# Optimization experiments

Measured on AMD Instinct MI355X. Metric: run time of the kernel, lower is better.

Reference implementation:

```python
import jax, jax.numpy as jnp
import numpy as np

B, L, IN_SIZE, EMB = 1024, 128, 64, 256
N_HEADS = 4
GAT_HID, GAT_HEADS = 64, 4
GAT_OUT = GAT_HEADS * GAT_HID  # 256 (concat=True)
NUM_CLASSES = 16
N_EDGES = 16384
NEG_SLOPE = 0.2


def layer_norm(x, g, b, eps=1e-5):
    mu = x.mean(-1, keepdims=True)
    var = x.var(-1, keepdims=True)
    return (x - mu) / jnp.sqrt(var + eps) * g + b


def mha(x, pad_mask, wqkv, bqkv, wo, bo):
    # torch nn.MultiheadAttention (batch_first), eval mode -> dropout is identity
    Bs, Ls, Em = x.shape
    dh = Em // N_HEADS
    qkv = x @ wqkv + bqkv                                   # [B,L,3E]
    q, k, v = jnp.split(qkv, 3, axis=-1)
    q = q.reshape(Bs, Ls, N_HEADS, dh)
    k = k.reshape(Bs, Ls, N_HEADS, dh)
    v = v.reshape(Bs, Ls, N_HEADS, dh)
    scores = jnp.einsum('bqhd,bkhd->bhqk', q, k) * (1.0 / np.sqrt(dh))
    scores = jnp.where(pad_mask[:, None, None, :], jnp.asarray(-1e9, scores.dtype), scores)
    attn = jax.nn.softmax(scores, axis=-1)
    out = jnp.einsum('bhqk,bkhd->bqhd', attn, v).reshape(Bs, Ls, Em)
    return out @ wo + bo


def gat_conv(h, src, dst, w, a_src, a_dst, bias):
    # PyG GATConv: per-node linear, additive attention, segment softmax over
    # incoming edges (grouped by dst), scatter-add aggregation, concat heads.
    N = h.shape[0]
    xh = (h @ w).reshape(N, GAT_HEADS, -1)                  # [N,H,F]
    s = (xh * a_src).sum(-1)                                # [N,H]
    d = (xh * a_dst).sum(-1)                                # [N,H]
    e = s[src] + d[dst]                                     # [E,H]
    e = jnp.where(e > 0, e, NEG_SLOPE * e)                  # leaky_relu(0.2)
    emax = jax.ops.segment_max(e, dst, num_segments=N)      # per-dst max
    ee = jnp.exp(e - emax[dst])
    denom = jax.ops.segment_sum(ee, dst, num_segments=N)
    coef = ee / (denom[dst] + 1e-16)                        # [E,H]
    msg = xh[src] * coef[:, :, None]                        # [E,H,F]
    out = jax.ops.segment_sum(msg, dst, num_segments=N)     # [N,H,F]
    return out.reshape(N, -1) + bias


def setup_inputs():
    key = jax.random.key(0)
    ks = jax.random.split(key, 16)
    rn = lambda i, shape, fan: jax.random.normal(ks[i], shape, jnp.float32) / np.sqrt(fan)
    inp = {}
    inp['x'] = jax.random.normal(ks[0], (B, L, IN_SIZE), jnp.float32)
    inp['lengths'] = jax.random.randint(ks[1], (B,), 1, L + 1)
    inp['edge_index'] = jax.random.randint(ks[2], (2, N_EDGES), 0, B)
    inp['in_w'] = rn(3, (IN_SIZE, EMB), IN_SIZE)
    inp['in_b'] = jnp.zeros((EMB,), jnp.float32)
    inp['mha1_wqkv'] = rn(4, (EMB, 3 * EMB), EMB)
    inp['mha1_bqkv'] = jnp.zeros((3 * EMB,), jnp.float32)
    inp['mha1_wo'] = rn(5, (EMB, EMB), EMB)
    inp['mha1_bo'] = jnp.zeros((EMB,), jnp.float32)
    inp['mha2_wqkv'] = rn(6, (EMB, 3 * EMB), EMB)
    inp['mha2_bqkv'] = jnp.zeros((3 * EMB,), jnp.float32)
    inp['mha2_wo'] = rn(7, (EMB, EMB), EMB)
    inp['mha2_bo'] = jnp.zeros((EMB,), jnp.float32)
    inp['ln1_g'] = jnp.ones((EMB,), jnp.float32)
    inp['ln1_b'] = jnp.zeros((EMB,), jnp.float32)
    inp['ln2_g'] = jnp.ones((EMB,), jnp.float32)
    inp['ln2_b'] = jnp.zeros((EMB,), jnp.float32)
    inp['gat1_w'] = rn(8, (EMB, GAT_OUT), EMB)
    inp['gat1_asrc'] = rn(9, (GAT_HEADS, GAT_HID), GAT_HID)
    inp['gat1_adst'] = rn(10, (GAT_HEADS, GAT_HID), GAT_HID)
    inp['gat1_bias'] = jnp.zeros((GAT_OUT,), jnp.float32)
    inp['gat2_w'] = rn(11, (GAT_OUT, GAT_OUT), GAT_OUT)
    inp['gat2_asrc'] = rn(12, (GAT_HEADS, GAT_HID), GAT_HID)
    inp['gat2_adst'] = rn(13, (GAT_HEADS, GAT_HID), GAT_HID)
    inp['gat2_bias'] = jnp.zeros((GAT_OUT,), jnp.float32)
    inp['lng1_g'] = jnp.ones((GAT_OUT,), jnp.float32)
    inp['lng1_b'] = jnp.zeros((GAT_OUT,), jnp.float32)
    inp['lng2_g'] = jnp.ones((GAT_OUT,), jnp.float32)
    inp['lng2_b'] = jnp.zeros((GAT_OUT,), jnp.float32)
    inp['fc_w'] = rn(14, (GAT_OUT, NUM_CLASSES), GAT_OUT)
    inp['fc_b'] = jnp.zeros((NUM_CLASSES,), jnp.float32)
    return inp


def reference(x, lengths, edge_index, in_w, in_b,
              mha1_wqkv, mha1_bqkv, mha1_wo, mha1_bo,
              mha2_wqkv, mha2_bqkv, mha2_wo, mha2_bo,
              ln1_g, ln1_b, ln2_g, ln2_b,
              gat1_w, gat1_asrc, gat1_adst, gat1_bias,
              gat2_w, gat2_asrc, gat2_adst, gat2_bias,
              lng1_g, lng1_b, lng2_g, lng2_b, fc_w, fc_b):
    pad_mask = jnp.arange(L)[None, :] >= lengths[:, None]   # True = padding
    h = x @ in_w + in_b                                     # [B,L,EMB]
    h = layer_norm(h + mha(h, pad_mask, mha1_wqkv, mha1_bqkv, mha1_wo, mha1_bo), ln1_g, ln1_b)
    h = layer_norm(h + mha(h, pad_mask, mha2_wqkv, mha2_bqkv, mha2_wo, mha2_bo), ln2_g, ln2_b)
    valid = (~pad_mask)[:, :, None].astype(h.dtype)
    pooled = (h * valid).sum(1) / jnp.clip(lengths, 1, None)[:, None].astype(h.dtype)  # [B,EMB]
    src, dst = edge_index[0], edge_index[1]
    g = gat_conv(pooled, src, dst, gat1_w, gat1_asrc, gat1_adst, gat1_bias)
    g = jax.nn.relu(layer_norm(g, lng1_g, lng1_b))
    g = gat_conv(g, src, dst, gat2_w, gat2_asrc, gat2_adst, gat2_bias)
    g = jax.nn.relu(layer_norm(g, lng2_g, lng2_b))
    return g @ fc_w + fc_b
```

## Files before the change

### kernel.cpp

```cpp
#include <hip/hip_runtime.h>
#include <hip/hip_bf16.h>
#include <cstdint>
#include <cstddef>

#define B_SZ    1024
#define L_SEQ   128
#define INSZ    64
#define EMB     256
#define NH      4
#define DH      64
#define QKV3    768
#define NEDGE   16384
#define GHEADS  4
#define GHID    64
#define GOUT    256
#define NCLS    16

#define NCHUNK     8
#define BCHUNK     (B_SZ / NCHUNK)
#define ROWS_CHUNK (BCHUNK * L_SEQ)

typedef unsigned short ushort_t;
typedef short bf16x8 __attribute__((ext_vector_type(8)));
typedef float f32x4 __attribute__((ext_vector_type(4)));
typedef ushort_t us4 __attribute__((ext_vector_type(4)));
typedef ushort_t us8 __attribute__((ext_vector_type(8)));

__device__ __forceinline__ ushort_t f32_to_bf16_rne(float x) {
    unsigned u = __float_as_uint(x);
    unsigned r = u + 0x7FFFu + ((u >> 16) & 1u);
    return (ushort_t)(r >> 16);
}
__device__ __forceinline__ float bf16u_to_f32(ushort_t h) {
    return __uint_as_float(((unsigned)h) << 16);
}

__global__ __launch_bounds__(256) void wsplit_kernel(
    const float* __restrict__ W, ushort_t* __restrict__ WtH,
    ushort_t* __restrict__ WtL, int K, int N)
{
    const int t = blockIdx.x * 256 + threadIdx.x;
    if (t >= K * N) return;
    const int n = t / K, k = t - n * K;
    const float x = W[(size_t)k * N + n];
    const ushort_t hi = f32_to_bf16_rne(x);
    const ushort_t lo = f32_to_bf16_rne(x - bf16u_to_f32(hi));
    WtH[t] = hi;
    WtL[t] = lo;
}

#define AKP 40

__global__ __launch_bounds__(256) void gemm_mfma_split(
    const float* __restrict__ A, const ushort_t* __restrict__ BtH,
    const ushort_t* __restrict__ BtL, const float* __restrict__ bias,
    float* __restrict__ C, int K, int lda, int ldc)
{
    __shared__ __attribute__((aligned(16))) ushort_t AsH[128][AKP];
    __shared__ __attribute__((aligned(16))) ushort_t AsL[128][AKP];
    __shared__ __attribute__((aligned(16))) ushort_t BsH[128][AKP];
    __shared__ __attribute__((aligned(16))) ushort_t BsL[128][AKP];

    const int tid  = threadIdx.x;
    const int lane = tid & 63;
    const int wv   = tid >> 6;
    const int wm   = (wv >> 1) << 6;
    const int wn   = (wv & 1) << 6;
    const int fr   = lane & 15;
    const int fk   = (lane >> 4) << 3;
    const size_t brow = (size_t)blockIdx.y << 7;
    const int    bcol = blockIdx.x << 7;

    const int ar = tid >> 3;
    const int ac = (tid & 7) << 2;
    const int bn = tid >> 1;
    const int bk = (tid & 1) << 4;

    f32x4 acc[4][4] = {};

    for (int k0 = 0; k0 < K; k0 += 32) {
        #pragma unroll
        for (int rr = 0; rr < 4; ++rr) {
            const int row = ar + (rr << 5);
            const float4 v = *reinterpret_cast<const float4*>(
                &A[(brow + row) * lda + k0 + ac]);
            const ushort_t h0 = f32_to_bf16_rne(v.x);
            const ushort_t h1 = f32_to_bf16_rne(v.y);
            const ushort_t h2 = f32_to_bf16_rne(v.z);
            const ushort_t h3 = f32_to_bf16_rne(v.w);
            const ushort_t l0 = f32_to_bf16_rne(v.x - bf16u_to_f32(h0));
            const ushort_t l1 = f32_to_bf16_rne(v.y - bf16u_to_f32(h1));
            const ushort_t l2 = f32_to_bf16_rne(v.z - bf16u_to_f32(h2));
            const ushort_t l3 = f32_to_bf16_rne(v.w - bf16u_to_f32(h3));
            us4 hv = {h0, h1, h2, h3};
            us4 lv = {l0, l1, l2, l3};
            *reinterpret_cast<us4*>(&AsH[row][ac]) = hv;
            *reinterpret_cast<us4*>(&AsL[row][ac]) = lv;
        }
        {
            const size_t bb = (size_t)(bcol + bn) * K + k0 + bk;
            *reinterpret_cast<us8*>(&BsH[bn][bk]) =
                *reinterpret_cast<const us8*>(&BtH[bb]);
            *reinterpret_cast<us8*>(&BsH[bn][bk + 8]) =
                *reinterpret_cast<const us8*>(&BtH[bb + 8]);
            *reinterpret_cast<us8*>(&BsL[bn][bk]) =
                *reinterpret_cast<const us8*>(&BtL[bb]);
            *reinterpret_cast<us8*>(&BsL[bn][bk + 8]) =
                *reinterpret_cast<const us8*>(&BtL[bb + 8]);
        }
        __syncthreads();

        bf16x8 aH[4], aL[4], bH[4], bL[4];
        #pragma unroll
        for (int i = 0; i < 4; ++i) {
            aH[i] = *reinterpret_cast<const bf16x8*>(&AsH[wm + (i << 4) + fr][fk]);
            aL[i] = *reinterpret_cast<const bf16x8*>(&AsL[wm + (i << 4) + fr][fk]);
            bH[i] = *reinterpret_cast<const bf16x8*>(&BsH[wn + (i << 4) + fr][fk]);
            bL[i] = *reinterpret_cast<const bf16x8*>(&BsL[wn + (i << 4) + fr][fk]);
        }
        #pragma unroll
        for (int i = 0; i < 4; ++i) {
            #pragma unroll
            for (int j = 0; j < 4; ++j) {
                acc[i][j] = __builtin_amdgcn_mfma_f32_16x16x32_bf16(
                    aH[i], bH[j], acc[i][j], 0, 0, 0);
                acc[i][j] = __builtin_amdgcn_mfma_f32_16x16x32_bf16(
                    aL[i], bH[j], acc[i][j], 0, 0, 0);
                acc[i][j] = __builtin_amdgcn_mfma_f32_16x16x32_bf16(
                    aH[i], bL[j], acc[i][j], 0, 0, 0);
            }
        }
        __syncthreads();
    }

    const int r4 = (lane >> 4) << 2;
    #pragma unroll
    for (int j = 0; j < 4; ++j) {
        const int col = bcol + wn + (j << 4) + fr;
        const float bv = bias ? bias[col] : 0.f;
        #pragma unroll
        for (int i = 0; i < 4; ++i) {
            #pragma unroll
            for (int r = 0; r < 4; ++r) {
                const size_t row = brow + wm + (i << 4) + r4 + r;
                C[row * ldc + col] = acc[i][j][r] + bv;
            }
        }
    }
}

#define BM 64
#define BN 64
#define BK 32

__global__ __launch_bounds__(256) void gemm_bias(
    const float* __restrict__ A, const float* __restrict__ Bm,
    const float* __restrict__ bias, float* __restrict__ C,
    int M, int N, int K, int lda, int ldb, int ldc)
{
    __shared__ float As[BK][BM + 4];
    __shared__ float Bs[BK][BN];
    const int tid = threadIdx.x;
    const int tx = tid & 15, ty = tid >> 4;
    const int brow = blockIdx.y * BM, bcol = blockIdx.x * BN;

    float acc[4][4] = {{0.f, 0.f, 0.f, 0.f}, {0.f, 0.f, 0.f, 0.f},
                       {0.f, 0.f, 0.f, 0.f}, {0.f, 0.f, 0.f, 0.f}};

    for (int k0 = 0; k0 < K; k0 += BK) {
        {
            const int r  = tid >> 3;
            const int c4 = (tid & 7) << 2;
            #pragma unroll
            for (int rr = 0; rr < 2; ++rr) {
                const int row = r + (rr << 5);
                const float4 v = *reinterpret_cast<const float4*>(
                    &A[(size_t)(brow + row) * lda + k0 + c4]);
                As[c4 + 0][row] = v.x;
                As[c4 + 1][row] = v.y;
                As[c4 + 2][row] = v.z;
                As[c4 + 3][row] = v.w;
            }
        }
        {
            const int r  = tid >> 4;
            const int c4 = tx << 2;
            #pragma unroll
            for (int rr = 0; rr < 2; ++rr) {
                const int row = r + (rr << 4);
                *reinterpret_cast<float4*>(&Bs[row][c4]) =
                    *reinterpret_cast<const float4*>(
                        &Bm[(size_t)(k0 + row) * ldb + bcol + c4]);
            }
        }
        __syncthreads();
        #pragma unroll
        for (int k = 0; k < BK; ++k) {
            const float4 av = *reinterpret_cast<const float4*>(&As[k][ty << 2]);
            const float4 bv = *reinterpret_cast<const float4*>(&Bs[k][tx << 2]);
            acc[0][0] += av.x * bv.x; acc[0][1] += av.x * bv.y;
            acc[0][2] += av.x * bv.z; acc[0][3] += av.x * bv.w;
            acc[1][0] += av.y * bv.x; acc[1][1] += av.y * bv.y;
            acc[1][2] += av.y * bv.z; acc[1][3] += av.y * bv.w;
            acc[2][0] += av.z * bv.x; acc[2][1] += av.z * bv.y;
            acc[2][2] += av.z * bv.z; acc[2][3] += av.z * bv.w;
            acc[3][0] += av.w * bv.x; acc[3][1] += av.w * bv.y;
            acc[3][2] += av.w * bv.z; acc[3][3] += av.w * bv.w;
        }
        __syncthreads();
    }

    float b0 = 0.f, b1 = 0.f, b2 = 0.f, b3 = 0.f;
    if (bias) {
        const int col = bcol + (tx << 2);
        b0 = bias[col]; b1 = bias[col + 1]; b2 = bias[col + 2]; b3 = bias[col + 3];
    }
    #pragma unroll
    for (int i = 0; i < 4; ++i) {
        const int row = brow + (ty << 2) + i;
        float4 o;
        o.x = acc[i][0] + b0; o.y = acc[i][1] + b1;
        o.z = acc[i][2] + b2; o.w = acc[i][3] + b3;
        *reinterpret_cast<float4*>(&C[(size_t)row * ldc + bcol + (tx << 2)]) = o;
    }
}

__global__ __launch_bounds__(256) void attn_kernel(
    const float* __restrict__ qkv, const int* __restrict__ lengths,
    float* __restrict__ out, int b0)
{
    const int bid = blockIdx.x;
    const int lb  = bid >> 4;
    const int h   = (bid >> 2) & 3;
    const int qc  = bid & 3;
    const int len = lengths[b0 + lb];
    const int tid = threadIdx.x;

    const size_t rowbase = (size_t)lb * L_SEQ;
    const int q0 = qc * 32;

    if (q0 >= len) {
        const int oi  = tid >> 3;
        const int oc0 = (tid & 7) << 3;
        float4 z = {0.f, 0.f, 0.f, 0.f};
        float* dst = &out[(rowbase + q0 + oi) * EMB + h * DH + oc0];
        *reinterpret_cast<float4*>(dst)     = z;
        *reinterpret_cast<float4*>(dst + 4) = z;
        return;
    }
    const int n_kc = (len + 31) >> 5;

    __shared__ float Qs[32][DH + 4];
    __shared__ float Kt[DH][36];
    __shared__ float Vs[32][DH + 4];
    __shared__ float Ss[32][L_SEQ + 4];

    {
        const int r  = tid >> 4;
        const int c4 = (tid & 15) << 2;
        #pragma unroll
        for (int rr = 0; rr < 2; ++rr) {
            const int row = r + (rr << 4);
            float4 v = *reinterpret_cast<const float4*>(
                &qkv[(rowbase + q0 + row) * QKV3 + h * DH + c4]);
            v.x *= 0.125f; v.y *= 0.125f; v.z *= 0.125f; v.w *= 0.125f;
            *reinterpret_cast<float4*>(&Qs[row][c4]) = v;
        }
    }

    for (int kc = 0; kc < n_kc; ++kc) {
        {
            const int r  = tid >> 4;
            const int c4 = (tid & 15) << 2;
            #pragma unroll
            for (int rr = 0; rr < 2; ++rr) {
                const int row = r + (rr << 4);
                const float4 v = *reinterpret_cast<const float4*>(
                    &qkv[(rowbase + kc * 32 + row) * QKV3 + EMB + h * DH + c4]);
                Kt[c4 + 0][row] = v.x;
                Kt[c4 + 1][row] = v.y;
                Kt[c4 + 2][row] = v.z;
                Kt[c4 + 3][row] = v.w;
            }
        }
        __syncthreads();
        const int si  = tid >> 3;
        const int sj0 = (tid & 7) << 2;
        float s0 = 0.f, s1 = 0.f, s2 = 0.f, s3 = 0.f;
        #pragma unroll
        for (int d = 0; d < DH; ++d) {
            const float qv = Qs[si][d];
            const float4 kv = *reinterpret_cast<const float4*>(&Kt[d][sj0]);
            s0 += qv * kv.x; s1 += qv * kv.y; s2 += qv * kv.z; s3 += qv * kv.w;
        }
        Ss[si][kc * 32 + sj0 + 0] = s0;
        Ss[si][kc * 32 + sj0 + 1] = s1;
        Ss[si][kc * 32 + sj0 + 2] = s2;
        Ss[si][kc * 32 + sj0 + 3] = s3;
        __syncthreads();
    }

    {
        const int r    = tid >> 3;
        const int lane = tid & 7;
        float m = -3.0e38f;
        #pragma unroll
        for (int jj = 0; jj < 16; ++jj) {
            const int j = lane + (jj << 3);
            if (j < len) m = fmaxf(m, Ss[r][j]);
        }
        #pragma unroll
        for (int o = 1; o < 8; o <<= 1) m = fmaxf(m, __shfl_xor(m, o, 8));
        float sum = 0.f;
        float ev[16];
        #pragma unroll
        for (int jj = 0; jj < 16; ++jj) {
            const int j = lane + (jj << 3);
            float e = 0.f;
            if (j < len) { e = __expf(Ss[r][j] - m); }
            ev[jj] = e;
            sum += e;
        }
        #pragma unroll
        for (int o = 1; o < 8; o <<= 1) sum += __shfl_xor(sum, o, 8);
        const float inv = 1.f / sum;
        #pragma unroll
        for (int jj = 0; jj < 16; ++jj) {
            const int j = lane + (jj << 3);
            Ss[r][j] = ev[jj] * inv;
        }
    }
    __syncthreads();

    const int oi  = tid >> 3;
    const int oc0 = (tid & 7) << 3;
    float o[8] = {0.f, 0.f, 0.f, 0.f, 0.f, 0.f, 0.f, 0.f};
    for (int kc = 0; kc < n_kc; ++kc) {
        {
            const int r  = tid >> 4;
            const int c4 = (tid & 15) << 2;
            #pragma unroll
            for (int rr = 0; rr < 2; ++rr) {
                const int row = r + (rr << 4);
                *reinterpret_cast<float4*>(&Vs[row][c4]) =
                    *reinterpret_cast<const float4*>(
                        &qkv[(rowbase + kc * 32 + row) * QKV3 + 2 * EMB + h * DH + c4]);
            }
        }
        __syncthreads();
        #pragma unroll
        for (int kk = 0; kk < 32; ++kk) {
            const float p = Ss[oi][kc * 32 + kk];
            const float4 v0 = *reinterpret_cast<const float4*>(&Vs[kk][oc0]);
            const float4 v1 = *reinterpret_cast<const float4*>(&Vs[kk][oc0 + 4]);
            o[0] += p * v0.x; o[1] += p * v0.y; o[2] += p * v0.z; o[3] += p * v0.w;
            o[4] += p * v1.x; o[5] += p * v1.y; o[6] += p * v1.z; o[7] += p * v1.w;
        }
        __syncthreads();
    }
    {
        float4 w0, w1;
        w0.x = o[0]; w0.y = o[1]; w0.z = o[2]; w0.w = o[3];
        w1.x = o[4]; w1.y = o[5]; w1.z = o[6]; w1.w = o[7];
        float* dst = &out[(rowbase + q0 + oi) * EMB + h * DH + oc0];
        *reinterpret_cast<float4*>(dst)     = w0;
        *reinterpret_cast<float4*>(dst + 4) = w1;
    }
}

__global__ __launch_bounds__(256) void ln_kernel(
    const float* __restrict__ x, const float* __restrict__ res,
    const float* __restrict__ bias, const float* __restrict__ g,
    const float* __restrict__ beta, float* __restrict__ out, int relu)
{
    const int lane = threadIdx.x & 63;
    const int w    = threadIdx.x >> 6;
    const size_t row = (size_t)blockIdx.x * 4 + w;
    const int c = lane << 2;

    float4 v = *reinterpret_cast<const float4*>(&x[row * 256 + c]);
    if (res) {
        const float4 r = *reinterpret_cast<const float4*>(&res[row * 256 + c]);
        v.x += r.x; v.y += r.y; v.z += r.z; v.w += r.w;
    }
    if (bias) {
        const float4 b = *reinterpret_cast<const float4*>(&bias[c]);
        v.x += b.x; v.y += b.y; v.z += b.z; v.w += b.w;
    }
    float s = v.x + v.y + v.z + v.w;
    #pragma unroll
    for (int o = 32; o >= 1; o >>= 1) s += __shfl_xor(s, o, 64);
    const float mu = s * (1.f / 256.f);
    const float dx = v.x - mu, dy = v.y - mu, dz = v.z - mu, dw = v.w - mu;
    float q = dx * dx + dy * dy + dz * dz + dw * dw;
    #pragma unroll
    for (int o = 32; o >= 1; o >>= 1) q += __shfl_xor(q, o, 64);
    const float rs = rsqrtf(q * (1.f / 256.f) + 1e-5f);
    const float4 gg = *reinterpret_cast<const float4*>(&g[c]);
    const float4 bb = *reinterpret_cast<const float4*>(&beta[c]);
    float4 o4;
    o4.x = dx * rs * gg.x + bb.x;
    o4.y = dy * rs * gg.y + bb.y;
    o4.z = dz * rs * gg.z + bb.z;
    o4.w = dw * rs * gg.w + bb.w;
    if (relu) {
        o4.x = fmaxf(o4.x, 0.f); o4.y = fmaxf(o4.y, 0.f);
        o4.z = fmaxf(o4.z, 0.f); o4.w = fmaxf(o4.w, 0.f);
    }
    *reinterpret_cast<float4*>(&out[row * 256 + c]) = o4;
}

__global__ __launch_bounds__(256) void pool_kernel(
    const float* __restrict__ h, const int* __restrict__ lengths,
    float* __restrict__ pooled)
{
    const int b = blockIdx.x;
    const int c = threadIdx.x;
    const int len = lengths[b];
    float s = 0.f;
    for (int l = 0; l < len; ++l)
        s += h[((size_t)b * L_SEQ + l) * EMB + c];
    pooled[(size_t)b * EMB + c] = s / (float)len;
}

__global__ __launch_bounds__(256) void gat_sd_kernel(
    const float* __restrict__ xh, const float* __restrict__ asrc,
    const float* __restrict__ adst, float* __restrict__ sbuf,
    float* __restrict__ dbuf)
{
    const int n  = blockIdx.x;
    const int hd = threadIdx.x >> 6;
    const int d  = threadIdx.x & 63;
    const float xv = xh[(size_t)n * GOUT + hd * GHID + d];
    float sv = xv * asrc[hd * GHID + d];
    float dv = xv * adst[hd * GHID + d];
    #pragma unroll
    for (int o = 32; o >= 1; o >>= 1) {
        sv += __shfl_down(sv, o, 64);
        dv += __shfl_down(dv, o, 64);
    }
    if (d == 0) {
        sbuf[n * GHEADS + hd] = sv;
        dbuf[n * GHEADS + hd] = dv;
    }
}

__global__ __launch_bounds__(256) void csr_count(
    const int* __restrict__ ei, int* __restrict__ deg)
{
    const int e = blockIdx.x * 256 + threadIdx.x;
    if (e < NEDGE) atomicAdd(&deg[ei[NEDGE + e]], 1);
}

__global__ __launch_bounds__(1024) void csr_scan(
    const int* __restrict__ deg, int* __restrict__ offs, int* __restrict__ cursor)
{
    __shared__ int tmp[1024];
    const int t = threadIdx.x;
    const int v = deg[t];
    tmp[t] = v;
    __syncthreads();
    #pragma unroll
    for (int o = 1; o < 1024; o <<= 1) {
        const int x = (t >= o) ? tmp[t - o] : 0;
        __syncthreads();
        tmp[t] += x;
        __syncthreads();
    }
    const int excl = tmp[t] - v;
    offs[t]   = excl;
    cursor[t] = excl;
    if (t == 1023) offs[1024] = tmp[1023];
}

__global__ __launch_bounds__(256) void csr_fill(
    const int* __restrict__ ei, int* __restrict__ cursor, int* __restrict__ esrc)
{
    const int e = blockIdx.x * 256 + threadIdx.x;
    if (e < NEDGE) {
        const int dst = ei[NEDGE + e];
        const int pos = atomicAdd(&cursor[dst], 1);
        esrc[pos] = ei[e];
    }
}

__global__ __launch_bounds__(256) void gat_gather(
    const int* __restrict__ esrc, const int* __restrict__ offs,
    const float* __restrict__ sbuf, const float* __restrict__ dbuf,
    const float* __restrict__ xh, float* __restrict__ outb)
{
    const int n = blockIdx.x;
    const int f = threadIdx.x;
    const int h = f >> 6;
    const int beg = offs[n], end = offs[n + 1];
    const float dv = dbuf[n * GHEADS + h];

    float m = -3.0e38f;
    for (int i = beg; i < end; ++i) {
        const int src = esrc[i];
        float e = sbuf[src * GHEADS + h] + dv;
        e = e > 0.f ? e : 0.2f * e;
        m = fmaxf(m, e);
    }
    float sum = 0.f, acc = 0.f;
    for (int i = beg; i < end; ++i) {
        const int src = esrc[i];
        float e = sbuf[src * GHEADS + h] + dv;
        e = e > 0.f ? e : 0.2f * e;
        const float ee = __expf(e - m);
        sum += ee;
        acc += ee * xh[(size_t)src * GOUT + f];
    }
    outb[(size_t)n * GOUT + f] = acc / (sum + 1e-16f);
}

__global__ __launch_bounds__(256) void fc_kernel(
    const float* __restrict__ g, const float* __restrict__ w,
    const float* __restrict__ b, float* __restrict__ out)
{
    const int node = blockIdx.x * 16 + (threadIdx.x >> 4);
    const int c    = threadIdx.x & 15;
    float s = 0.f;
    for (int k = 0; k < 256; ++k)
        s += g[(size_t)node * 256 + k] * w[k * NCLS + c];
    out[node * NCLS + c] = s + b[c];
}

extern "C" void kernel_launch(void* const* d_in, const int* in_sizes, int n_in,
                              void* d_out, int out_size, void* d_ws, size_t ws_size,
                              hipStream_t stream)
{
    const float* x        = (const float*)d_in[0];
    const int*   lengths  = (const int*)d_in[1];
    const int*   eidx     = (const int*)d_in[2];
    const float* in_w     = (const float*)d_in[3];
    const float* in_b     = (const float*)d_in[4];
    const float* wqkv[2]  = {(const float*)d_in[5], (const float*)d_in[9]};
    const float* bqkv[2]  = {(const float*)d_in[6], (const float*)d_in[10]};
    const float* wo[2]    = {(const float*)d_in[7], (const float*)d_in[11]};
    const float* bo[2]    = {(const float*)d_in[8], (const float*)d_in[12]};
    const float* ln_g[2]  = {(const float*)d_in[13], (const float*)d_in[15]};
    const float* ln_b[2]  = {(const float*)d_in[14], (const float*)d_in[16]};
    const float* gat_w[2]    = {(const float*)d_in[17], (const float*)d_in[21]};
    const float* gat_asrc[2] = {(const float*)d_in[18], (const float*)d_in[22]};
    const float* gat_adst[2] = {(const float*)d_in[19], (const float*)d_in[23]};
    const float* gat_bias[2] = {(const float*)d_in[20], (const float*)d_in[24]};
    const float* lng_g[2] = {(const float*)d_in[25], (const float*)d_in[27]};
    const float* lng_b[2] = {(const float*)d_in[26], (const float*)d_in[28]};
    const float* fc_w     = (const float*)d_in[29];
    const float* fc_b     = (const float*)d_in[30];
    float* outp = (float*)d_out;

    float* W = (float*)d_ws;
    float* Hbuf   = W;
    float* QKVc   = Hbuf + (size_t)33554432;
    float* Ac     = QKVc + (size_t)12582912;
    float* Pc     = Ac   + (size_t)4194304;
    float* pooled = Pc   + (size_t)4194304;
    float* xh     = pooled + (size_t)262144;
    float* g1     = xh   + (size_t)262144;
    float* gacc   = g1   + (size_t)262144;
    float* sbuf   = gacc + (size_t)262144;
    float* dbuf   = sbuf + 4096;
    int* deg    = (int*)(dbuf + 4096);
    int* offs   = deg + 1024;
    int* cursor = offs + 1056;
    int* esrc   = cursor + 1024;
    ushort_t* us = (ushort_t*)(esrc + 16384);
    ushort_t* inwtH   = us;
    ushort_t* inwtL   = inwtH + 16384;
    ushort_t* qkvtH0  = inwtL + 16384;
    ushort_t* qkvtL0  = qkvtH0 + 196608;
    ushort_t* qkvtH1  = qkvtL0 + 196608;
    ushort_t* qkvtL1  = qkvtH1 + 196608;
    ushort_t* wotH0   = qkvtL1 + 196608;
    ushort_t* wotL0   = wotH0 + 65536;
    ushort_t* wotH1   = wotL0 + 65536;
    ushort_t* wotL1   = wotH1 + 65536;
    ushort_t* qkvtH[2] = {qkvtH0, qkvtH1};
    ushort_t* qkvtL[2] = {qkvtL0, qkvtL1};
    ushort_t* wotH[2]  = {wotH0, wotH1};
    ushort_t* wotL[2]  = {wotL0, wotL1};

    wsplit_kernel<<<(INSZ * EMB + 255) / 256, 256, 0, stream>>>(
        in_w, inwtH, inwtL, INSZ, EMB);
    for (int l = 0; l < 2; ++l) {
        wsplit_kernel<<<(EMB * QKV3 + 255) / 256, 256, 0, stream>>>(
            wqkv[l], qkvtH[l], qkvtL[l], EMB, QKV3);
        wsplit_kernel<<<(EMB * EMB + 255) / 256, 256, 0, stream>>>(
            wo[l], wotH[l], wotL[l], EMB, EMB);
    }

    hipMemsetAsync(deg, 0, 1024 * sizeof(int), stream);
    csr_count<<<NEDGE / 256, 256, 0, stream>>>(eidx, deg);
    csr_scan<<<1, 1024, 0, stream>>>(deg, offs, cursor);
    csr_fill<<<NEDGE / 256, 256, 0, stream>>>(eidx, cursor, esrc);

    gemm_mfma_split<<<dim3(EMB / 128, (B_SZ * L_SEQ) / 128), 256, 0, stream>>>(
        x, inwtH, inwtL, in_b, Hbuf, INSZ, INSZ, EMB);

    for (int layer = 0; layer < 2; ++layer) {
        for (int ck = 0; ck < NCHUNK; ++ck) {
            float* Hc = Hbuf + (size_t)ck * ROWS_CHUNK * EMB;
            gemm_mfma_split<<<dim3(QKV3 / 128, ROWS_CHUNK / 128), 256, 0, stream>>>(
                Hc, qkvtH[layer], qkvtL[layer], bqkv[layer], QKVc,
                EMB, EMB, QKV3);
            attn_kernel<<<BCHUNK * NH * 4, 256, 0, stream>>>(
                QKVc, lengths, Ac, ck * BCHUNK);
            gemm_mfma_split<<<dim3(EMB / 128, ROWS_CHUNK / 128), 256, 0, stream>>>(
                Ac, wotH[layer], wotL[layer], bo[layer], Pc,
                EMB, EMB, EMB);
            ln_kernel<<<ROWS_CHUNK / 4, 256, 0, stream>>>(
                Hc, Pc, nullptr, ln_g[layer], ln_b[layer], Hc, 0);
        }
    }

    pool_kernel<<<B_SZ, 256, 0, stream>>>(Hbuf, lengths, pooled);

    const float* gin = pooled;
    float* gout_ln[2] = {g1, pooled};
    for (int layer = 0; layer < 2; ++layer) {
        gemm_bias<<<dim3(GOUT / BN, B_SZ / BM), 256, 0, stream>>>(
            gin, gat_w[layer], nullptr, xh, B_SZ, GOUT, GOUT, GOUT, GOUT, GOUT);
        gat_sd_kernel<<<B_SZ, 256, 0, stream>>>(
            xh, gat_asrc[layer], gat_adst[layer], sbuf, dbuf);
        gat_gather<<<B_SZ, 256, 0, stream>>>(
            esrc, offs, sbuf, dbuf, xh, gacc);
        ln_kernel<<<B_SZ / 4, 256, 0, stream>>>(
            gacc, nullptr, gat_bias[layer], lng_g[layer], lng_b[layer],
            gout_ln[layer], 1);
        gin = gout_ln[layer];
    }

    fc_kernel<<<B_SZ / 16, 256, 0, stream>>>(pooled, fc_w, fc_b, outp);
}
```

Baseline: 2.078 ms.

## Template split-bf16 MFMA GEMM on tile size, remap blocks per XCD, stage epilogue

Turns the split-bf16 MFMA GEMM into a template over block tile sizes and launches smaller tiles (128x64 and 64x64) so each launch has more workgroups. It also remaps workgroup IDs so neighbouring tiles land on the same XCD for better L2 reuse. The output goes through shared memory, which reuses the staging buffer, so stores are coalesced float4 writes with the bias add. Smaller tiles give less data reuse per block, and the staged epilogue adds extra barriers.

After: 1.991 ms. 1.04x faster.

```diff
diff --git a/kernel.cpp b/kernel.cpp
--- a/kernel.cpp
+++ b/kernel.cpp
@@ -51,37 +51,56 @@
 
 #define AKP 40
 
-__global__ __launch_bounds__(256) void gemm_mfma_split(
+template<int TBM, int TBN>
+__global__ __launch_bounds__(256) void gemm_mfma_split_t(
     const float* __restrict__ A, const ushort_t* __restrict__ BtH,
     const ushort_t* __restrict__ BtL, const float* __restrict__ bias,
     float* __restrict__ C, int K, int lda, int ldc)
 {
-    __shared__ __attribute__((aligned(16))) ushort_t AsH[128][AKP];
-    __shared__ __attribute__((aligned(16))) ushort_t AsL[128][AKP];
-    __shared__ __attribute__((aligned(16))) ushort_t BsH[128][AKP];
-    __shared__ __attribute__((aligned(16))) ushort_t BsL[128][AKP];
+    constexpr int A_EL  = TBM * AKP;
+    constexpr int B_EL  = TBN * AKP;
+    constexpr int CLDW  = TBN + 4;
+    constexpr int STAGE_BYTES = (2 * A_EL + 2 * B_EL) * 2;
+    constexpr int CST_BYTES   = 64 * CLDW * 4;
+    constexpr int RAW_BYTES   = STAGE_BYTES > CST_BYTES ? STAGE_BYTES : CST_BYTES;
+    __shared__ __attribute__((aligned(16))) char raw[RAW_BYTES];
+    ushort_t* AsH = (ushort_t*)raw;
+    ushort_t* AsL = AsH + A_EL;
+    ushort_t* BsH = AsL + A_EL;
+    ushort_t* BsL = BsH + B_EL;
+    float*    Cst = (float*)raw;
 
     const int tid  = threadIdx.x;
     const int lane = tid & 63;
     const int wv   = tid >> 6;
-    const int wm   = (wv >> 1) << 6;
-    const int wn   = (wv & 1) << 6;
+    const int wm   = (wv >> 1) * (TBM / 2);
+    const int wn   = (wv & 1) * (TBN / 2);
     const int fr   = lane & 15;
     const int fk   = (lane >> 4) << 3;
-    const size_t brow = (size_t)blockIdx.y << 7;
-    const int    bcol = blockIdx.x << 7;
-
-    const int ar = tid >> 3;
-    const int ac = (tid & 7) << 2;
-    const int bn = tid >> 1;
-    const int bk = (tid & 1) << 4;
-
-    f32x4 acc[4][4] = {};
+    constexpr int MI = TBM / 32;
+    constexpr int NJ = TBN / 32;
+
+    const int nwg  = gridDim.x * gridDim.y;
+    const int orig = blockIdx.y * gridDim.x + blockIdx.x;
+    const int q8 = nwg >> 3, r8 = nwg & 7;
+    const int xcd = orig & 7, lid = orig >> 3;
+    const int wgid = (xcd < r8 ? xcd * (q8 + 1) : r8 * (q8 + 1) + (xcd - r8) * q8) + lid;
+    const int bx = wgid % gridDim.x;
+    const int by = wgid / gridDim.x;
+    const size_t brow = (size_t)by * TBM;
+    const int    bcol = bx * TBN;
+
+    const int ar  = tid >> 3;
+    const int ac  = (tid & 7) << 2;
+    const int brn = tid >> 2;
+    const int bk  = (tid & 3) << 3;
+
+    f32x4 acc[MI][NJ] = {};
 
     for (int k0 = 0; k0 < K; k0 += 32) {
         #pragma unroll
-        for (int rr = 0; rr < 4; ++rr) {
-            const int row = ar + (rr << 5);
+        for (int p = 0; p < TBM / 32; ++p) {
+            const int row = p * 32 + ar;
             const float4 v = *reinterpret_cast<const float4*>(
                 &A[(brow + row) * lda + k0 + ac]);
             const ushort_t h0 = f32_to_bf16_rne(v.x);
@@ -94,34 +113,35 @@
             const ushort_t l3 = f32_to_bf16_rne(v.w - bf16u_to_f32(h3));
             us4 hv = {h0, h1, h2, h3};
             us4 lv = {l0, l1, l2, l3};
-            *reinterpret_cast<us4*>(&AsH[row][ac]) = hv;
-            *reinterpret_cast<us4*>(&AsL[row][ac]) = lv;
-        }
-        {
-            const size_t bb = (size_t)(bcol + bn) * K + k0 + bk;
-            *reinterpret_cast<us8*>(&BsH[bn][bk]) =
+            *reinterpret_cast<us4*>(&AsH[row * AKP + ac]) = hv;
+            *reinterpret_cast<us4*>(&AsL[row * AKP + ac]) = lv;
+        }
+        #pragma unroll
+        for (int p = 0; p < TBN / 64; ++p) {
+            const int row = p * 64 + brn;
+            const size_t bb = (size_t)(bcol + row) * K + k0 + bk;
+            *reinterpret_cast<us8*>(&BsH[row * AKP + bk]) =
                 *reinterpret_cast<const us8*>(&BtH[bb]);
-            *reinterpret_cast<us8*>(&BsH[bn][bk + 8]) =
-                *reinterpret_cast<const us8*>(&BtH[bb + 8]);
-            *reinterpret_cast<us8*>(&BsL[bn][bk]) =
+            *reinterpret_cast<us8*>(&BsL[row * AKP + bk]) =
                 *reinterpret_cast<const us8*>(&BtL[bb]);
-            *reinterpret_cast<us8*>(&BsL[bn][bk + 8]) =
-                *reinterpret_cast<const us8*>(&BtL[bb + 8]);
-        }
-        __syncthreads();
-
-        bf16x8 aH[4], aL[4], bH[4], bL[4];
-        #pragma unroll
-        for (int i = 0; i < 4; ++i) {
-            aH[i] = *reinterpret_cast<const bf16x8*>(&AsH[wm + (i << 4) + fr][fk]);
-            aL[i] = *reinterpret_cast<const bf16x8*>(&AsL[wm + (i << 4) + fr][fk]);
-            bH[i] = *reinterpret_cast<const bf16x8*>(&BsH[wn + (i << 4) + fr][fk]);
-            bL[i] = *reinterpret_cast<const bf16x8*>(&BsL[wn + (i << 4) + fr][fk]);
-        }
-        #pragma unroll
-        for (int i = 0; i < 4; ++i) {
+        }
+        __syncthreads();
+
+        bf16x8 aH[MI], aL[MI], bH[NJ], bL[NJ];
+        #pragma unroll
+        for (int i = 0; i < MI; ++i) {
+            aH[i] = *reinterpret_cast<const bf16x8*>(&AsH[(wm + (i << 4) + fr) * AKP + fk]);
+            aL[i] = *reinterpret_cast<const bf16x8*>(&AsL[(wm + (i << 4) + fr) * AKP + fk]);
+        }
+        #pragma unroll
+        for (int j = 0; j < NJ; ++j) {
+            bH[j] = *reinterpret_cast<const bf16x8*>(&BsH[(wn + (j << 4) + fr) * AKP + fk]);
+            bL[j] = *reinterpret_cast<const bf16x8*>(&BsL[(wn + (j << 4) + fr) * AKP + fk]);
+        }
+        #pragma unroll
+        for (int i = 0; i < MI; ++i) {
             #pragma unroll
-            for (int j = 0; j < 4; ++j) {
+            for (int j = 0; j < NJ; ++j) {
                 acc[i][j] = __builtin_amdgcn_mfma_f32_16x16x32_bf16(
                     aH[i], bH[j], acc[i][j], 0, 0, 0);
                 acc[i][j] = __builtin_amdgcn_mfma_f32_16x16x32_bf16(
@@ -135,16 +155,33 @@
 
     const int r4 = (lane >> 4) << 2;
     #pragma unroll
-    for (int j = 0; j < 4; ++j) {
-        const int col = bcol + wn + (j << 4) + fr;
-        const float bv = bias ? bias[col] : 0.f;
-        #pragma unroll
-        for (int i = 0; i < 4; ++i) {
+    for (int g = 0; g < TBM / 64; ++g) {
+        __syncthreads();
+        if (wm / 64 == g) {
             #pragma unroll
-            for (int r = 0; r < 4; ++r) {
-                const size_t row = brow + wm + (i << 4) + r4 + r;
-                C[row * ldc + col] = acc[i][j][r] + bv;
+            for (int i = 0; i < MI; ++i)
+                #pragma unroll
+                for (int j = 0; j < NJ; ++j)
+                    #pragma unroll
+                    for (int r = 0; r < 4; ++r)
+                        Cst[(wm - g * 64 + (i << 4) + r4 + r) * CLDW
+                            + wn + (j << 4) + fr] = acc[i][j][r];
+        }
+        __syncthreads();
+        constexpr int F4R = TBN / 4;
+        constexpr int NF4 = 64 * F4R / 256;
+        #pragma unroll
+        for (int p = 0; p < NF4; ++p) {
+            const int idx  = p * 256 + tid;
+            const int row  = idx / F4R;
+            const int colf = (idx % F4R) * 4;
+            float4 v = *reinterpret_cast<const float4*>(&Cst[row * CLDW + colf]);
+            if (bias) {
+                const float4 bv = *reinterpret_cast<const float4*>(&bias[bcol + colf]);
+                v.x += bv.x; v.y += bv.y; v.z += bv.z; v.w += bv.w;
             }
+            *reinterpret_cast<float4*>(
+                &C[(brow + g * 64 + row) * ldc + bcol + colf]) = v;
         }
     }
 }
@@ -596,18 +633,18 @@
     csr_scan<<<1, 1024, 0, stream>>>(deg, offs, cursor);
     csr_fill<<<NEDGE / 256, 256, 0, stream>>>(eidx, cursor, esrc);
 
-    gemm_mfma_split<<<dim3(EMB / 128, (B_SZ * L_SEQ) / 128), 256, 0, stream>>>(
+    gemm_mfma_split_t<128, 64><<<dim3(EMB / 64, (B_SZ * L_SEQ) / 128), 256, 0, stream>>>(
         x, inwtH, inwtL, in_b, Hbuf, INSZ, INSZ, EMB);
 
     for (int layer = 0; layer < 2; ++layer) {
         for (int ck = 0; ck < NCHUNK; ++ck) {
             float* Hc = Hbuf + (size_t)ck * ROWS_CHUNK * EMB;
-            gemm_mfma_split<<<dim3(QKV3 / 128, ROWS_CHUNK / 128), 256, 0, stream>>>(
+            gemm_mfma_split_t<128, 64><<<dim3(QKV3 / 64, ROWS_CHUNK / 128), 256, 0, stream>>>(
                 Hc, qkvtH[layer], qkvtL[layer], bqkv[layer], QKVc,
                 EMB, EMB, QKV3);
             attn_kernel<<<BCHUNK * NH * 4, 256, 0, stream>>>(
                 QKVc, lengths, Ac, ck * BCHUNK);
-            gemm_mfma_split<<<dim3(EMB / 128, ROWS_CHUNK / 128), 256, 0, stream>>>(
+            gemm_mfma_split_t<64, 64><<<dim3(EMB / 64, ROWS_CHUNK / 64), 256, 0, stream>>>(
                 Ac, wotH[layer], wotL[layer], bo[layer], Pc,
                 EMB, EMB, EMB);
             ln_kernel<<<ROWS_CHUNK / 4, 256, 0, stream>>>(
```
